# Kernel tuning notes

Hardware: AMD Instinct MI355X
Metric: run time of the kernel (lower is better)

The kernel has to match this reference:

```python
import jax, jax.numpy as jnp
import numpy as np
from math import sqrt

HEAD_DIM = 128
MASKED = True


def setup_inputs() -> dict:
    key = jax.random.key(0)
    kq, kk, kv = jax.random.split(key, 3)
    B, S, D = 16, 2048, HEAD_DIM
    return {
        "queries": jax.random.normal(kq, (B, S, D), dtype=jnp.float32),
        "keys": jax.random.normal(kk, (B, S, D), dtype=jnp.float32),
        "values": jax.random.normal(kv, (B, S, D), dtype=jnp.float32),
    }


def reference(queries, keys, values):
    # scores: (B, Sq, Sk)
    scores = jnp.einsum("bqd,bkd->bqk", queries, keys) / sqrt(HEAD_DIM)
    if MASKED:
        # Faithful to torch.tril: upper-triangular entries set to 0.0
        # (NOT -inf) BEFORE softmax — reproduces the original's
        # multiplicative mask semantics exactly.
        scores = jnp.tril(scores)
    weights = jax.nn.softmax(scores, axis=-1)
    return jnp.einsum("bqk,bkd->bqd", weights, values)
```

## Files before the change

kernel.cpp:

```cpp
#include <hip/hip_runtime.h>
#include <hip/hip_bf16.h>

#define DEVI static __device__ __forceinline__

typedef __attribute__((ext_vector_type(8))) short short8;
typedef __attribute__((ext_vector_type(16))) float f32x16;

#define S_LEN 2048
#define D_DIM 128
#define NBATCH 16
#define QSC ((float)(0.08838834764831845 * 1.4426950408889634))

#if __has_builtin(__builtin_amdgcn_exp2f)
#define EXP2(x) __builtin_amdgcn_exp2f(x)
#else
#define EXP2(x) exp2f(x)
#endif

DEVI unsigned short f2bf(float x) {
  union { float f; unsigned int u; } a; a.f = x;
  unsigned int u = a.u;
  unsigned int r = (u + 0x7fffu + ((u >> 16) & 1u)) >> 16;
  return (unsigned short)r;
}

DEVI unsigned int cvtpk(float lo, float hi) {
  unsigned int r;
  asm volatile("v_cvt_pk_bf16_f32 %0, %1, %2" : "=v"(r) : "v"(lo), "v"(hi));
  return r;
}


__global__ void cvtk(const float* __restrict__ K, unsigned short* __restrict__ Kb) {
  const int M4 = (NBATCH * S_LEN * D_DIM) / 4;
  for (int i = blockIdx.x * blockDim.x + threadIdx.x; i < M4;
       i += gridDim.x * blockDim.x) {
    const size_t idx = (size_t)i * 4;
    const float4 v = *reinterpret_cast<const float4*>(K + idx);
    ushort4 o;
    o.x = f2bf(v.x); o.y = f2bf(v.y); o.z = f2bf(v.z); o.w = f2bf(v.w);
    *reinterpret_cast<ushort4*>(Kb + idx) = o;
  }
}

__global__ void vtrans(const float* __restrict__ V, unsigned short* __restrict__ Vt,
                       float* __restrict__ Tsum) {
  __shared__ unsigned short t[64][68];
  const int bid = blockIdx.x;
  const int b = bid >> 6, rem = bid & 63;
  const int st = rem & 31, s0 = st * 64, d0 = (rem >> 5) * 64;
  const int tt = threadIdx.x;
  const int r = tt >> 2, c = (tt & 3) * 16;
  const float* src = V + ((size_t)(b * S_LEN + s0 + r)) * D_DIM + d0 + c;
#pragma unroll
  for (int i = 0; i < 4; i++) {
    float4 v = reinterpret_cast<const float4*>(src)[i];
    t[r][c + 4 * i + 0] = f2bf(v.x);
    t[r][c + 4 * i + 1] = f2bf(v.y);
    t[r][c + 4 * i + 2] = f2bf(v.z);
    t[r][c + 4 * i + 3] = f2bf(v.w);
  }
  __syncthreads();
  unsigned short* dst = Vt + ((size_t)(b * D_DIM + d0 + r)) * S_LEN + s0 + c;
#pragma unroll
  for (int i = 0; i < 4; i++) {
    ushort4 o;
    o.x = t[c + 4 * i + 0][r];
    o.y = t[c + 4 * i + 1][r];
    o.z = t[c + 4 * i + 2][r];
    o.w = t[c + 4 * i + 3][r];
    reinterpret_cast<ushort4*>(dst)[i] = o;
  }
  if (tt < 64) {
    float s = 0.0f;
#pragma unroll 8
    for (int rr = 0; rr < 64; rr++) {
      union { float f; unsigned int u; } cv;
      cv.u = ((unsigned int)t[rr][tt]) << 16;
      s += cv.f;
    }
    Tsum[((size_t)b * 32 + st) * 128 + d0 + tt] = s;
  }
}

__global__ void sufB(const float* __restrict__ Tsum, float* __restrict__ SufV) {
  const int b = blockIdx.x;
  const int d = threadIdx.x;
  float run = 0.0f;
  SufV[((size_t)b * 33 + 32) * 128 + d] = 0.0f;
  for (int t = 31; t >= 0; t--) {
    run += Tsum[((size_t)b * 32 + t) * 128 + d];
    SufV[((size_t)b * 33 + t) * 128 + d] = run;
  }
}


DEVI void stage_tiles(char* ldsK, char* ldsV, const unsigned short* Kb,
                      const unsigned short* Vt, int b, int kt, int w, int lane) {
  const int kv0 = kt * 64;
  if (w < 2) {
    const char* ktile = (const char*)(Kb + ((size_t)b * S_LEN + kv0) * D_DIM);
#pragma unroll
    for (int i = 0; i < 8; i++) {
      int c = w * 8 + i;
      int L = c * 1024 + lane * 16;
      int row = L >> 8;
      int src = row * 256 + ((L & 255) ^ ((row & 7) << 4));
      __builtin_amdgcn_global_load_lds(
          (const __attribute__((address_space(1))) unsigned int*)(ktile + src),
          (__attribute__((address_space(3))) unsigned int*)(ldsK + c * 1024),
          16, 0, 0);
    }
  } else {
#pragma unroll
    for (int i = 0; i < 8; i++) {
      int c = (w - 2) * 8 + i;
      int L = c * 1024 + lane * 16;
      int row = L >> 7;
      int xs = (L & 127) ^ ((row & 7) << 4);
      const char* src = (const char*)Vt +
                        (((size_t)b * D_DIM + row) * S_LEN + kv0) * 2 + xs;
      __builtin_amdgcn_global_load_lds(
          (const __attribute__((address_space(1))) unsigned int*)src,
          (__attribute__((address_space(3))) unsigned int*)(ldsV + c * 1024),
          16, 0, 0);
    }
  }
}

DEVI short8 ldK(const char* ldsK, int row, int off) {
  int addr = row * 256 + (off ^ ((row & 7) << 4));
  return *reinterpret_cast<const short8*>(ldsK + addr);
}
DEVI short8 ldV(const char* ldsV, int row, int off) {
  int addr = row * 128 + (off ^ ((row & 7) << 4));
  return *reinterpret_cast<const short8*>(ldsV + addr);
}

template <bool MASK>
DEVI void tile_body(const char* cb, const short8* qf, f32x16 (&acc)[4],
                    float& m_run, float& l_run, const int ln31, const int h,
                    const int kh, const int qrow, const int kvb) {
  f32x16 sT;
#pragma unroll
  for (int r = 0; r < 16; r++) sT[r] = 0.0f;
#pragma unroll
  for (int kf = 0; kf < 8; kf++) {
    short8 af = ldK(cb, ln31 + 32 * kh, 32 * kf + 16 * h);
    sT = __builtin_amdgcn_mfma_f32_32x32x16_bf16(af, qf[kf], sT, 0, 0, 0);
  }
  if (MASK) {
#pragma unroll
    for (int r = 0; r < 16; r++) {
      int kvg = kvb + (r & 3) + 8 * (r >> 2) + 4 * h;
      if (kvg > qrow) sT[r] = 0.0f;
    }
  }
  float tm[8];
#pragma unroll
  for (int r = 0; r < 8; r++) tm[r] = fmaxf(sT[r], sT[r + 8]);
#pragma unroll
  for (int r = 0; r < 4; r++) tm[r] = fmaxf(tm[r], tm[r + 4]);
  float mx = fmaxf(fmaxf(tm[0], tm[2]), fmaxf(tm[1], tm[3]));
  mx = fmaxf(mx, __shfl_xor(mx, 32));
  if (!__all(mx <= m_run + 8.0f)) {
    float mnew = fmaxf(m_run, mx);
    float alpha = EXP2(m_run - mnew);
    m_run = mnew;
    l_run *= alpha;
    float ar[16];
#pragma unroll
    for (int r = 0; r < 16; r++)
      ar[r] = __shfl(alpha, (r & 3) + 8 * (r >> 2) + 4 * h);
#pragma unroll
    for (int nt = 0; nt < 4; nt++)
#pragma unroll
      for (int r = 0; r < 16; r++) acc[nt][r] *= ar[r];
  }
#pragma unroll
  for (int r = 0; r < 16; r++) sT[r] = EXP2(sT[r] - m_run);
  float ts[8];
#pragma unroll
  for (int r = 0; r < 8; r++) ts[r] = sT[r] + sT[r + 8];
#pragma unroll
  for (int r = 0; r < 4; r++) ts[r] = ts[r] + ts[r + 4];
  float sum = (ts[0] + ts[1]) + (ts[2] + ts[3]);
  sum += __shfl_xor(sum, 32);
  l_run += sum;
#pragma unroll
  for (int kl = 0; kl < 2; kl++) {
    const int ra = 4 * (2 * kl);
    const int rb = 4 * (2 * kl + 1);
    unsigned int ua0 = cvtpk(sT[ra + 0], sT[ra + 1]);
    unsigned int ua1 = cvtpk(sT[ra + 2], sT[ra + 3]);
    unsigned int ub0 = cvtpk(sT[rb + 0], sT[rb + 1]);
    unsigned int ub1 = cvtpk(sT[rb + 2], sT[rb + 3]);
    unsigned int uloc0 = h ? ub0 : ua0, uloc1 = h ? ub1 : ua1;
    unsigned int usnd0 = h ? ua0 : ub0, usnd1 = h ? ua1 : ub1;
    unsigned int urcv0 = (unsigned int)__shfl_xor((int)usnd0, 32);
    unsigned int urcv1 = (unsigned int)__shfl_xor((int)usnd1, 32);
    union { short8 v; unsigned int u[4]; } pa;
    pa.u[0] = h ? urcv0 : uloc0;
    pa.u[1] = h ? urcv1 : uloc1;
    pa.u[2] = h ? uloc0 : urcv0;
    pa.u[3] = h ? uloc1 : urcv1;
    const int vboff = 64 * kh + 32 * kl + 16 * h;
#pragma unroll
    for (int nt = 0; nt < 4; nt++) {
      short8 vb = ldV(cb + 16384, ln31 + 32 * nt, vboff);
      acc[nt] = __builtin_amdgcn_mfma_f32_32x32x16_bf16(pa.v, vb, acc[nt], 0, 0, 0);
    }
  }
}

__global__ __launch_bounds__(256, 2) void attn_kernel(
    const float* __restrict__ Q, const unsigned short* __restrict__ Kb,
    const unsigned short* __restrict__ Vt, const float* __restrict__ SufV,
    float* __restrict__ out) {
  __shared__ __align__(16) char smem[2][32768];

  const int tid = threadIdx.x;
  const int w = tid >> 6, lane = tid & 63;
  const int ln31 = lane & 31, h = lane >> 5;
  const int qs = w & 1;
  const int kh = w >> 1;

  const int bid = blockIdx.x;
  const int x = bid & 7, s = bid >> 3;
  const int b = 2 * x + (s & 1);
  const int sh = s >> 1;
  const int j = (s < 32) ? sh : (47 - sh);
  const int q0 = j * 64;
  const int kv_end = q0 + 64;
  const int qrow = q0 + 32 * qs + ln31;

  short8 qf[8];
  {
    const float* qsrc = Q + ((size_t)b * S_LEN + qrow) * D_DIM + 8 * h;
#pragma unroll
    for (int kf = 0; kf < 8; kf++) {
      float4 a = *reinterpret_cast<const float4*>(qsrc + 16 * kf);
      float4 c = *reinterpret_cast<const float4*>(qsrc + 16 * kf + 4);
      union { short8 v; unsigned int u[4]; } q8;
      q8.u[0] = cvtpk(a.x * QSC, a.y * QSC);
      q8.u[1] = cvtpk(a.z * QSC, a.w * QSC);
      q8.u[2] = cvtpk(c.x * QSC, c.y * QSC);
      q8.u[3] = cvtpk(c.z * QSC, c.w * QSC);
      qf[kf] = q8.v;
    }
  }

  f32x16 acc[4];
#pragma unroll
  for (int nt = 0; nt < 4; nt++)
#pragma unroll
    for (int r = 0; r < 16; r++) acc[nt][r] = 0.0f;

  float m_run = 0.0f, l_run = 0.0f;

  stage_tiles(smem[0], smem[0] + 16384, Kb, Vt, b, 0, w, lane);
  __syncthreads();

  for (int kt = 0; kt < j; kt++) {
    char* cb = smem[kt & 1];
    stage_tiles(smem[(kt + 1) & 1], smem[(kt + 1) & 1] + 16384, Kb, Vt, b,
                kt + 1, w, lane);
    tile_body<false>(cb, qf, acc, m_run, l_run, ln31, h, kh, qrow,
                     kt * 64 + 32 * kh);
    __syncthreads();
  }
  tile_body<true>(smem[j & 1], qf, acc, m_run, l_run, ln31, h, kh, qrow,
                  j * 64 + 32 * kh);
  __syncthreads();

  float* mb = (float*)smem;
  if (kh == 1) {
    float* p = mb + (size_t)(qs * 64 + lane) * 69;
#pragma unroll
    for (int nt = 0; nt < 4; nt++)
#pragma unroll
      for (int r = 0; r < 16; r++) p[nt * 16 + r] = acc[nt][r];
    p[64] = m_run;
    p[65] = l_run;
  }
  __syncthreads();
  if (kh == 0) {
    const float* p = mb + (size_t)(qs * 64 + lane) * 69;
    float m1 = p[64], l1 = p[65];
    float m12 = fmaxf(m_run, m1);
    float b0 = EXP2(m_run - m12);
    float b1 = EXP2(m1 - m12);
    float l12 = l_run * b0 + l1 * b1;
    float e = EXP2(-m12);
    l12 += (float)(S_LEN - kv_end) * e;
    float b0r[16], b1r[16], er[16], lr[16];
#pragma unroll
    for (int r = 0; r < 16; r++) {
      int cr = (r & 3) + 8 * (r >> 2) + 4 * h;
      b0r[r] = __shfl(b0, cr);
      b1r[r] = __shfl(b1, cr);
      er[r] = __shfl(e, cr);
      lr[r] = __shfl(l12, cr);
    }
    const float* sv = SufV + ((size_t)b * 33 + (kv_end >> 6)) * 128;
    float* ob = out + ((size_t)b * S_LEN + q0 + 32 * qs) * D_DIM + ln31;
#pragma unroll
    for (int nt = 0; nt < 4; nt++) {
      float svv = sv[ln31 + 32 * nt];
#pragma unroll
      for (int r = 0; r < 16; r++) {
        int cr = (r & 3) + 8 * (r >> 2) + 4 * h;
        float o = acc[nt][r] * b0r[r] + p[nt * 16 + r] * b1r[r] + er[r] * svv;
        ob[(size_t)cr * D_DIM + 32 * nt] = o / lr[r];
      }
    }
  }
}


extern "C" void kernel_launch(void* const* d_in, const int* in_sizes, int n_in,
                              void* d_out, int out_size, void* d_ws, size_t ws_size,
                              hipStream_t stream) {
  const float* Q = (const float*)d_in[0];
  const float* K = (const float*)d_in[1];
  const float* V = (const float*)d_in[2];
  float* out = (float*)d_out;

  char* ws = (char*)d_ws;
  unsigned short* Kb = (unsigned short*)ws;
  unsigned short* Vt = Kb + 4194304;
  float* Tsum = (float*)(ws + 16777216);
  float* SufV = Tsum + 65536;

  cvtk<<<2048, 256, 0, stream>>>(K, Kb);
  vtrans<<<1024, 256, 0, stream>>>(V, Vt, Tsum);
  sufB<<<16, 128, 0, stream>>>(Tsum, SufV);
  attn_kernel<<<512, 256, 0, stream>>>(Q, Kb, Vt, SufV, out);
}
```

Baseline: 64.78 us.

## Pair causal strips per block, fuse prep kernels, use permlane32 swaps

Each attention block now handles two complementary query strips (31-p and p) in sequence, giving every block equal causal work. The grid halves to 256 blocks and launch bounds drop to one block per CU. The K and V preprocessing kernels merge into a single launch, and sufB loads its inputs up front. Cross-half shuffles are replaced with permlane32_swap, and the K LDS swizzle widens to 16 rows. The risk is lower occupancy and less overlap between strips, since each block runs its two strips serially.

```diff
diff --git a/kernel.cpp b/kernel.cpp
--- a/kernel.cpp
+++ b/kernel.cpp
@@ -5,6 +5,7 @@
 
 typedef __attribute__((ext_vector_type(8))) short short8;
 typedef __attribute__((ext_vector_type(16))) float f32x16;
+typedef __attribute__((ext_vector_type(2))) unsigned int uintx2;
 
 #define S_LEN 2048
 #define D_DIM 128
@@ -30,26 +31,46 @@
   return r;
 }
 
-
-__global__ void cvtk(const float* __restrict__ K, unsigned short* __restrict__ Kb) {
-  const int M4 = (NBATCH * S_LEN * D_DIM) / 4;
-  for (int i = blockIdx.x * blockDim.x + threadIdx.x; i < M4;
-       i += gridDim.x * blockDim.x) {
-    const size_t idx = (size_t)i * 4;
-    const float4 v = *reinterpret_cast<const float4*>(K + idx);
-    ushort4 o;
-    o.x = f2bf(v.x); o.y = f2bf(v.y); o.z = f2bf(v.z); o.w = f2bf(v.w);
-    *reinterpret_cast<ushort4*>(Kb + idx) = o;
-  }
-}
-
-__global__ void vtrans(const float* __restrict__ V, unsigned short* __restrict__ Vt,
-                       float* __restrict__ Tsum) {
+DEVI void plswap(unsigned int& a, unsigned int& b) {
+  uintx2 r = __builtin_amdgcn_permlane32_swap(a, b, false, false);
+  a = r[0];
+  b = r[1];
+}
+
+DEVI float xhalf_max(float x) {
+  union { float f; unsigned int u; } a, b;
+  a.f = x; b.f = x;
+  plswap(a.u, b.u);
+  return fmaxf(a.f, b.f);
+}
+
+DEVI float xhalf_sum(float x) {
+  union { float f; unsigned int u; } a, b;
+  a.f = x; b.f = x;
+  plswap(a.u, b.u);
+  return a.f + b.f;
+}
+
+
+__global__ void prep(const float* __restrict__ K, const float* __restrict__ V,
+                     unsigned short* __restrict__ Kb, unsigned short* __restrict__ Vt,
+                     float* __restrict__ Tsum) {
   __shared__ unsigned short t[64][68];
+  const int tt = threadIdx.x;
+  if (blockIdx.x >= 1024) {
+    const int M4 = (NBATCH * S_LEN * D_DIM) / 4;
+    for (int i = (blockIdx.x - 1024) * 256 + tt; i < M4; i += 2048 * 256) {
+      const size_t idx = (size_t)i * 4;
+      const float4 v = *reinterpret_cast<const float4*>(K + idx);
+      ushort4 o;
+      o.x = f2bf(v.x); o.y = f2bf(v.y); o.z = f2bf(v.z); o.w = f2bf(v.w);
+      *reinterpret_cast<ushort4*>(Kb + idx) = o;
+    }
+    return;
+  }
   const int bid = blockIdx.x;
   const int b = bid >> 6, rem = bid & 63;
   const int st = rem & 31, s0 = st * 64, d0 = (rem >> 5) * 64;
-  const int tt = threadIdx.x;
   const int r = tt >> 2, c = (tt & 3) * 16;
   const float* src = V + ((size_t)(b * S_LEN + s0 + r)) * D_DIM + d0 + c;
 #pragma unroll
@@ -86,16 +107,20 @@
 __global__ void sufB(const float* __restrict__ Tsum, float* __restrict__ SufV) {
   const int b = blockIdx.x;
   const int d = threadIdx.x;
+  float v[32];
+#pragma unroll
+  for (int t = 0; t < 32; t++) v[t] = Tsum[((size_t)b * 32 + t) * 128 + d];
   float run = 0.0f;
   SufV[((size_t)b * 33 + 32) * 128 + d] = 0.0f;
+#pragma unroll
   for (int t = 31; t >= 0; t--) {
-    run += Tsum[((size_t)b * 32 + t) * 128 + d];
+    run += v[t];
     SufV[((size_t)b * 33 + t) * 128 + d] = run;
   }
 }
 
 
-DEVI void stage_tiles(char* ldsK, char* ldsV, const unsigned short* Kb,
+DEVI void stage_tiles(char* ldsbuf, const unsigned short* Kb,
                       const unsigned short* Vt, int b, int kt, int w, int lane) {
   const int kv0 = kt * 64;
   if (w < 2) {
@@ -105,13 +130,14 @@
       int c = w * 8 + i;
       int L = c * 1024 + lane * 16;
       int row = L >> 8;
-      int src = row * 256 + ((L & 255) ^ ((row & 7) << 4));
+      int src = row * 256 + ((L & 255) ^ ((row & 15) << 4));
       __builtin_amdgcn_global_load_lds(
           (const __attribute__((address_space(1))) unsigned int*)(ktile + src),
-          (__attribute__((address_space(3))) unsigned int*)(ldsK + c * 1024),
+          (__attribute__((address_space(3))) unsigned int*)(ldsbuf + c * 1024),
           16, 0, 0);
     }
   } else {
+    char* ldsV = ldsbuf + 16384;
 #pragma unroll
     for (int i = 0; i < 8; i++) {
       int c = (w - 2) * 8 + i;
@@ -129,7 +155,7 @@
 }
 
 DEVI short8 ldK(const char* ldsK, int row, int off) {
-  int addr = row * 256 + (off ^ ((row & 7) << 4));
+  int addr = row * 256 + (off ^ ((row & 15) << 4));
   return *reinterpret_cast<const short8*>(ldsK + addr);
 }
 DEVI short8 ldV(const char* ldsV, int row, int off) {
@@ -162,7 +188,7 @@
 #pragma unroll
   for (int r = 0; r < 4; r++) tm[r] = fmaxf(tm[r], tm[r + 4]);
   float mx = fmaxf(fmaxf(tm[0], tm[2]), fmaxf(tm[1], tm[3]));
-  mx = fmaxf(mx, __shfl_xor(mx, 32));
+  mx = xhalf_max(mx);
   if (!__all(mx <= m_run + 8.0f)) {
     float mnew = fmaxf(m_run, mx);
     float alpha = EXP2(m_run - mnew);
@@ -185,25 +211,20 @@
 #pragma unroll
   for (int r = 0; r < 4; r++) ts[r] = ts[r] + ts[r + 4];
   float sum = (ts[0] + ts[1]) + (ts[2] + ts[3]);
-  sum += __shfl_xor(sum, 32);
+  sum = xhalf_sum(sum);
   l_run += sum;
 #pragma unroll
   for (int kl = 0; kl < 2; kl++) {
-    const int ra = 4 * (2 * kl);
-    const int rb = 4 * (2 * kl + 1);
-    unsigned int ua0 = cvtpk(sT[ra + 0], sT[ra + 1]);
-    unsigned int ua1 = cvtpk(sT[ra + 2], sT[ra + 3]);
-    unsigned int ub0 = cvtpk(sT[rb + 0], sT[rb + 1]);
-    unsigned int ub1 = cvtpk(sT[rb + 2], sT[rb + 3]);
-    unsigned int uloc0 = h ? ub0 : ua0, uloc1 = h ? ub1 : ua1;
-    unsigned int usnd0 = h ? ua0 : ub0, usnd1 = h ? ua1 : ub1;
-    unsigned int urcv0 = (unsigned int)__shfl_xor((int)usnd0, 32);
-    unsigned int urcv1 = (unsigned int)__shfl_xor((int)usnd1, 32);
+    const int ra = 8 * kl;
+    const int rb = 8 * kl + 4;
+    unsigned int a0 = cvtpk(sT[ra + 0], sT[ra + 1]);
+    unsigned int a1 = cvtpk(sT[ra + 2], sT[ra + 3]);
+    unsigned int b0 = cvtpk(sT[rb + 0], sT[rb + 1]);
+    unsigned int b1 = cvtpk(sT[rb + 2], sT[rb + 3]);
+    plswap(a0, b0);
+    plswap(a1, b1);
     union { short8 v; unsigned int u[4]; } pa;
-    pa.u[0] = h ? urcv0 : uloc0;
-    pa.u[1] = h ? urcv1 : uloc1;
-    pa.u[2] = h ? uloc0 : urcv0;
-    pa.u[3] = h ? uloc1 : urcv1;
+    pa.u[0] = a0; pa.u[1] = a1; pa.u[2] = b0; pa.u[3] = b1;
     const int vboff = 64 * kh + 32 * kl + 16 * h;
 #pragma unroll
     for (int nt = 0; nt < 4; nt++) {
@@ -213,65 +234,39 @@
   }
 }
 
-__global__ __launch_bounds__(256, 2) void attn_kernel(
-    const float* __restrict__ Q, const unsigned short* __restrict__ Kb,
-    const unsigned short* __restrict__ Vt, const float* __restrict__ SufV,
-    float* __restrict__ out) {
-  __shared__ __align__(16) char smem[2][32768];
-
-  const int tid = threadIdx.x;
-  const int w = tid >> 6, lane = tid & 63;
-  const int ln31 = lane & 31, h = lane >> 5;
-  const int qs = w & 1;
-  const int kh = w >> 1;
-
-  const int bid = blockIdx.x;
-  const int x = bid & 7, s = bid >> 3;
-  const int b = 2 * x + (s & 1);
-  const int sh = s >> 1;
-  const int j = (s < 32) ? sh : (47 - sh);
+DEVI void run_strip(int j, int b, const short8 (&qf)[8], char* smem,
+                    const unsigned short* __restrict__ Kb,
+                    const unsigned short* __restrict__ Vt,
+                    const float* __restrict__ SufV, float* __restrict__ out,
+                    int w, int lane, int ln31, int h, int qs, int kh) {
   const int q0 = j * 64;
   const int kv_end = q0 + 64;
   const int qrow = q0 + 32 * qs + ln31;
 
-  short8 qf[8];
-  {
-    const float* qsrc = Q + ((size_t)b * S_LEN + qrow) * D_DIM + 8 * h;
-#pragma unroll
-    for (int kf = 0; kf < 8; kf++) {
-      float4 a = *reinterpret_cast<const float4*>(qsrc + 16 * kf);
-      float4 c = *reinterpret_cast<const float4*>(qsrc + 16 * kf + 4);
-      union { short8 v; unsigned int u[4]; } q8;
-      q8.u[0] = cvtpk(a.x * QSC, a.y * QSC);
-      q8.u[1] = cvtpk(a.z * QSC, a.w * QSC);
-      q8.u[2] = cvtpk(c.x * QSC, c.y * QSC);
-      q8.u[3] = cvtpk(c.z * QSC, c.w * QSC);
-      qf[kf] = q8.v;
-    }
-  }
-
   f32x16 acc[4];
 #pragma unroll
   for (int nt = 0; nt < 4; nt++)
 #pragma unroll
     for (int r = 0; r < 16; r++) acc[nt][r] = 0.0f;
-
   float m_run = 0.0f, l_run = 0.0f;
 
-  stage_tiles(smem[0], smem[0] + 16384, Kb, Vt, b, 0, w, lane);
+  stage_tiles(smem, Kb, Vt, b, 0, w, lane);
   __syncthreads();
-
-  for (int kt = 0; kt < j; kt++) {
-    char* cb = smem[kt & 1];
-    stage_tiles(smem[(kt + 1) & 1], smem[(kt + 1) & 1] + 16384, Kb, Vt, b,
-                kt + 1, w, lane);
-    tile_body<false>(cb, qf, acc, m_run, l_run, ln31, h, kh, qrow,
-                     kt * 64 + 32 * kh);
+  int cur = 0;
+  for (int kt = 0; kt <= j; kt++) {
+    char* cb = smem + (size_t)cur * 32768;
+    const int nxt = cur ^ 1;
+    if (kt < j) {
+      stage_tiles(smem + (size_t)nxt * 32768, Kb, Vt, b, kt + 1, w, lane);
+      tile_body<false>(cb, qf, acc, m_run, l_run, ln31, h, kh, qrow,
+                       kt * 64 + 32 * kh);
+    } else {
+      tile_body<true>(cb, qf, acc, m_run, l_run, ln31, h, kh, qrow,
+                      kt * 64 + 32 * kh);
+    }
     __syncthreads();
-  }
-  tile_body<true>(smem[j & 1], qf, acc, m_run, l_run, ln31, h, kh, qrow,
-                  j * 64 + 32 * kh);
-  __syncthreads();
+    cur = nxt;
+  }
 
   float* mb = (float*)smem;
   if (kh == 1) {
@@ -315,6 +310,47 @@
       }
     }
   }
+  __syncthreads();
+}
+
+__global__ __launch_bounds__(256, 1) void attn_kernel(
+    const float* __restrict__ Q, const unsigned short* __restrict__ Kb,
+    const unsigned short* __restrict__ Vt, const float* __restrict__ SufV,
+    float* __restrict__ out) {
+  __shared__ __align__(16) char smem[2 * 32768];
+
+  const int tid = threadIdx.x;
+  const int w = tid >> 6, lane = tid & 63;
+  const int ln31 = lane & 31, h = lane >> 5;
+  const int qs = w & 1;
+  const int kh = w >> 1;
+
+  const int bid = blockIdx.x;
+  const int x = bid & 7, idx = bid >> 3;
+  const int b = 2 * x + (idx & 1);
+  const int p = idx >> 1;
+
+  short8 qf[2][8];
+#pragma unroll
+  for (int si = 0; si < 2; si++) {
+    const int jj = si ? p : (31 - p);
+    const int qrow = jj * 64 + 32 * qs + ln31;
+    const float* qsrc = Q + ((size_t)b * S_LEN + qrow) * D_DIM + 8 * h;
+#pragma unroll
+    for (int kf = 0; kf < 8; kf++) {
+      float4 a = *reinterpret_cast<const float4*>(qsrc + 16 * kf);
+      float4 c = *reinterpret_cast<const float4*>(qsrc + 16 * kf + 4);
+      union { short8 v; unsigned int u[4]; } q8;
+      q8.u[0] = cvtpk(a.x * QSC, a.y * QSC);
+      q8.u[1] = cvtpk(a.z * QSC, a.w * QSC);
+      q8.u[2] = cvtpk(c.x * QSC, c.y * QSC);
+      q8.u[3] = cvtpk(c.z * QSC, c.w * QSC);
+      qf[si][kf] = q8.v;
+    }
+  }
+
+  run_strip(31 - p, b, qf[0], smem, Kb, Vt, SufV, out, w, lane, ln31, h, qs, kh);
+  run_strip(p, b, qf[1], smem, Kb, Vt, SufV, out, w, lane, ln31, h, qs, kh);
 }
 
 
@@ -332,8 +368,7 @@
   float* Tsum = (float*)(ws + 16777216);
   float* SufV = Tsum + 65536;
 
-  cvtk<<<2048, 256, 0, stream>>>(K, Kb);
-  vtrans<<<1024, 256, 0, stream>>>(V, Vt, Tsum);
+  prep<<<3072, 256, 0, stream>>>(K, V, Kb, Vt, Tsum);
   sufB<<<16, 128, 0, stream>>>(Tsum, SufV);
-  attn_kernel<<<512, 256, 0, stream>>>(Q, Kb, Vt, SufV, out);
-}
+  attn_kernel<<<256, 256, 0, stream>>>(Q, Kb, Vt, SufV, out);
+}
```

After: 75.62 us. +16.7%, slower.
